# Performance work log

Measured on AMD Instinct MI355X. Metric: run time of the kernel, lower is better.

The kernel has to match this reference:

```python
import jax, jax.numpy as jnp
import numpy as np

B, N, CS, CZ, CH, H, PQ, PV = 1, 768, 384, 128, 16, 12, 4, 8
INF, EPS, LN_EPS = 1e5, 1e-8, 1e-5


def setup_inputs() -> dict:
    key = jax.random.key(0)
    ks = jax.random.split(key, 16)
    def nrm(k, shape, scale=0.02):
        return jax.random.normal(k, shape, dtype=jnp.float32) * scale
    return {
        "s": jax.random.normal(ks[0], (B, N, CS), jnp.float32),
        "z": jax.random.normal(ks[1], (B, N, N, CZ), jnp.float32),
        "r_rot": jax.random.normal(ks[2], (B, N, 5, 3, 3), jnp.float32),
        "r_trans": jax.random.normal(ks[3], (B, N, 5, 3), jnp.float32),
        "mask": jnp.ones((B, N, 5), jnp.float32),
        "wq": nrm(ks[4], (H * CH, CS)), "bq": jnp.zeros((H * CH,), jnp.float32),
        "wkv": nrm(ks[5], (2 * H * CH, CS)), "bkv": jnp.zeros((2 * H * CH,), jnp.float32),
        "wqp": nrm(ks[6], (H * PQ * 3, CS)), "bqp": jnp.zeros((H * PQ * 3,), jnp.float32),
        "wkvp": nrm(ks[7], (H * (PQ + PV) * 3, CS)), "bkvp": jnp.zeros((H * (PQ + PV) * 3,), jnp.float32),
        "wb": nrm(ks[8], (H, CZ)), "bb": jnp.zeros((H,), jnp.float32),
        "head_w": nrm(ks[9], (H,), 0.5),
        "wout": nrm(ks[10], (CS, H * (CZ + CH + PV * 4))), "bout": jnp.zeros((CS,), jnp.float32),
        "wexp": nrm(ks[11], (5 * CS, CS)), "bexp": jnp.zeros((5 * CS,), jnp.float32),
        "ln_g": jnp.ones((CS,), jnp.float32), "ln_b": jnp.zeros((CS,), jnp.float32),
        "ww": nrm(ks[12], (1, CS)), "bw": jnp.zeros((1,), jnp.float32),
    }


def _mix(x, fg_mask, weight, ndims):
    # x: [B,N,5,...]; weighted blend of backbone frame (index 0) and mean of
    # masked functional-group frames (indices 1:5).
    bb_f = x[:, :, :1]
    m = fg_mask.reshape(fg_mask.shape + (1,) * ndims)
    fg = (x[:, :, 1:] * m).sum(axis=2, keepdims=True)
    denom = fg_mask.sum(-1, keepdims=True).reshape(fg_mask.shape[:2] + (1,) * (ndims + 1))
    fg = fg / (denom + 1e-8)
    w = weight.reshape(weight.shape[:2] + (1,) * (ndims + 1))
    return (w * bb_f + (1.0 - w) * fg)[:, :, 0]


def _ipa(s, z, r_rot, r_trans, mask, wq, bq, wkv, bkv, wqp, bqp, wkvp, bkvp,
         wb, bb, head_w, wout, bout, wexp, bexp, ln_g, ln_b, ww, bw):
    fg_mask = mask[..., 1:]            # [B,N,4]
    ulr = mask[..., 0]                 # [B,N]
    # softmax over a size-1 axis (as in original code -> all ones)
    weight = jax.nn.softmax(s @ ww.T + bw, axis=-1)   # [B,N,1]

    se = (s @ wexp.T + bexp).reshape(B, N, 5, CS)
    mu = se.mean(-1, keepdims=True)
    var = ((se - mu) ** 2).mean(-1, keepdims=True)
    se = (se - mu) * jax.lax.rsqrt(var + LN_EPS) * ln_g + ln_b

    q = _mix((se @ wq.T + bq).reshape(B, N, 5, H, CH), fg_mask, weight, 2)      # [B,N,H,CH]
    kv = _mix((se @ wkv.T + bkv).reshape(B, N, 5, H, 2 * CH), fg_mask, weight, 2)
    k, v = kv[..., :CH], kv[..., CH:]

    def pts_of(w_, b_, npts):
        lin = se @ w_.T + b_                                   # [B,N,5,3*H*npts]
        pts = jnp.moveaxis(lin.reshape(B, N, 5, 3, H * npts), -2, -1)  # [B,N,5,H*npts,3]
        pts = jnp.einsum('bnfij,bnfpj->bnfpi', r_rot, pts) + r_trans[:, :, :, None, :]
        return _mix(pts.reshape(B, N, 5, H, npts, 3), fg_mask, weight, 3)

    q_pts = pts_of(wqp, bqp, PQ)                               # [B,N,H,PQ,3]
    kv_pts = pts_of(wkvp, bkvp, PQ + PV)
    k_pts, v_pts = kv_pts[..., :PQ, :], kv_pts[..., PQ:, :]

    bias = z @ wb.T + bb                                       # [B,N,N,H]
    a = jnp.einsum('bihc,bjhc->bhij', q, k) * (1.0 / (3 * CH)) ** 0.5
    a = a + (1.0 / 3.0) ** 0.5 * jnp.transpose(bias, (0, 3, 1, 2))

    d2 = jnp.sum((q_pts[:, :, None] - k_pts[:, None]) ** 2, axis=-1)  # [B,N,N,H,PQ]
    hw = jax.nn.softplus(head_w) * (1.0 / (3 * (PQ * 9.0 / 2))) ** 0.5
    pt_att = -0.5 * jnp.sum(d2 * hw[:, None], axis=-1)         # [B,N,N,H]
    a = a + jnp.transpose(pt_att, (0, 3, 1, 2))
    sq_mask = INF * (ulr[:, :, None] * ulr[:, None, :] - 1.0)
    a = jax.nn.softmax(a + sq_mask[:, None], axis=-1)          # [B,H,N,N]

    o = jnp.einsum('bhij,bjhc->bihc', a, v).reshape(B, N, H * CH)
    o_pt = jnp.einsum('bhij,bjhpx->bihpx', a, v_pts)           # [B,N,H,PV,3]
    rot0, t0 = r_rot[:, :, 0], r_trans[:, :, 0]                # backbone frame
    # invert_apply: R^T (x - t)
    o_pt = jnp.einsum('bnik,bnhpi->bnhpk', rot0, o_pt - t0[:, :, None, None, :])
    o_pt_norm = jnp.sqrt(jnp.sum(o_pt ** 2, -1) + EPS).reshape(B, N, H * PV)
    o_pt = o_pt.reshape(B, N, H * PV, 3)
    o_pair = jnp.einsum('bhij,bijc->bihc', a, z).reshape(B, N, H * CZ)
    cat = jnp.concatenate([o, o_pt[..., 0], o_pt[..., 1], o_pt[..., 2], o_pt_norm, o_pair], -1)
    return cat @ wout.T + bout                                 # [B,N,CS]


def reference(s, z, r_rot, r_trans, mask, wq, bq, wkv, bkv, wqp, bqp, wkvp, bkvp,
              wb, bb, head_w, wout, bout, wexp, bexp, ln_g, ln_b, ww, bw):
    return _ipa(s, z, r_rot, r_trans, mask, wq, bq, wkv, bkv, wqp, bqp, wkvp, bkvp,
                wb, bb, head_w, wout, bout, wexp, bexp, ln_g, ln_b, ww, bw)
```

## Files before the change

### kernel.cpp

```cpp
#include <hip/hip_runtime.h>
#include <hip/hip_bf16.h>
#include <stdint.h>


typedef float  f32x4 __attribute__((ext_vector_type(4)));
typedef short  s16x8 __attribute__((ext_vector_type(8)));

__device__ __forceinline__ float bf2f(unsigned short u) {
    union { unsigned int i; float f; } v; v.i = ((unsigned int)u) << 16; return v.f;
}
__device__ __forceinline__ unsigned short f2bf(float f) {
    union { float f; unsigned int i; } v; v.f = f;
    unsigned int r = v.i + 0x7fffu + ((v.i >> 16) & 1u);
    return (unsigned short)(r >> 16);
}
__device__ __forceinline__ unsigned packbf2(float a, float b) {
    return (unsigned)f2bf(a) | ((unsigned)f2bf(b) << 16);
}
__device__ __forceinline__ float bval(int c,
    const float* bq, const float* bkv, const float* bqp, const float* bkvp)
{
    if (c < 192)      return bq[c];
    else if (c < 576) return bkv[c - 192];
    else if (c < 720) return bqp[c - 576];
    else              return bkvp[c - 720];
}

__global__ __launch_bounds__(256) void k_prep(
    const float* __restrict__ s, const float* __restrict__ wexp,
    const float* __restrict__ wq, const float* __restrict__ wkv,
    const float* __restrict__ wqp, const float* __restrict__ wkvp,
    const float* __restrict__ wout,
    const float* __restrict__ bq, const float* __restrict__ bkv,
    const float* __restrict__ bqp, const float* __restrict__ bkvp,
    unsigned short* __restrict__ s_bf, unsigned short* __restrict__ we_bf,
    unsigned short* __restrict__ wc_bf, unsigned short* __restrict__ wo_bf,
    float* __restrict__ bcat)
{
    const int x = blockIdx.x * 256 + threadIdx.x;
    if (x >= 1696896) return;
    if (x < 294912)            s_bf[x] = f2bf(s[x]);
    else if (x < 442368)       we_bf[x - 294912] = f2bf(wexp[x - 294912]);
    else if (x < 516096)       wc_bf[x - 442368] = f2bf(wq[x - 442368]);
    else if (x < 663552)       wc_bf[73728 + (x - 516096)] = f2bf(wkv[x - 516096]);
    else if (x < 718848)       wc_bf[221184 + (x - 663552)] = f2bf(wqp[x - 663552]);
    else if (x < 884736)       wc_bf[276480 + (x - 718848)] = f2bf(wkvp[x - 718848]);
    else if (x < 1695744)      wo_bf[x - 884736] = f2bf(wout[x - 884736]);
    else {
        int j = x - 1695744;
        bcat[j] = bval(j, bq, bkv, bqp, bkvp);
    }
}

__global__ __launch_bounds__(256) void k_mm(
    const unsigned short* __restrict__ A, int lda,
    const unsigned short* __restrict__ B, int ldb,
    float* __restrict__ C, int ldc, const float* __restrict__ bias,
    int nk, size_t pstride)
{
    const int m0 = blockIdx.x * 64, n0 = blockIdx.y * 64;
    const int koff = blockIdx.z * nk * 32;
    C += (size_t)blockIdx.z * pstride;
    const int t = threadIdx.x;
    const int lane = t & 63, wave = t >> 6, quad = lane >> 4, lcol = lane & 15;
    const int mh = (wave & 1) * 32, nh = (wave >> 1) * 32;
    __shared__ unsigned short As[64 * 40];
    __shared__ unsigned short Bs[64 * 40];
    const int lr = t >> 2, ls = (t & 3) * 8;
    const unsigned short* Ap = A + (size_t)(m0 + lr) * lda + koff + ls;
    const unsigned short* Bp = B + (size_t)(n0 + lr) * ldb + koff + ls;
    f32x4 acc[2][2] = {};

    uint4 av = *(const uint4*)Ap;
    uint4 bv = *(const uint4*)Bp;
    for (int kc = 0; kc < nk; ++kc) {
        __syncthreads();
        *(uint4*)&As[lr * 40 + ls] = av;
        *(uint4*)&Bs[lr * 40 + ls] = bv;
        __syncthreads();
        if (kc + 1 < nk) {
            av = *(const uint4*)(Ap + (size_t)(kc + 1) * 32);
            bv = *(const uint4*)(Bp + (size_t)(kc + 1) * 32);
        }
        s16x8 af0 = *(const s16x8*)&As[(mh + lcol) * 40 + quad * 8];
        s16x8 af1 = *(const s16x8*)&As[(mh + 16 + lcol) * 40 + quad * 8];
        s16x8 bf0 = *(const s16x8*)&Bs[(nh + lcol) * 40 + quad * 8];
        s16x8 bf1 = *(const s16x8*)&Bs[(nh + 16 + lcol) * 40 + quad * 8];
        acc[0][0] = __builtin_amdgcn_mfma_f32_16x16x32_bf16(af0, bf0, acc[0][0], 0, 0, 0);
        acc[0][1] = __builtin_amdgcn_mfma_f32_16x16x32_bf16(af0, bf1, acc[0][1], 0, 0, 0);
        acc[1][0] = __builtin_amdgcn_mfma_f32_16x16x32_bf16(af1, bf0, acc[1][0], 0, 0, 0);
        acc[1][1] = __builtin_amdgcn_mfma_f32_16x16x32_bf16(af1, bf1, acc[1][1], 0, 0, 0);
    }
    #pragma unroll
    for (int r = 0; r < 2; ++r)
        #pragma unroll
        for (int c = 0; c < 2; ++c) {
            int gn = n0 + nh + c * 16 + lcol;
            float bv2 = bias ? bias[gn] : 0.f;
            #pragma unroll
            for (int ii = 0; ii < 4; ++ii) {
                int gm = m0 + mh + r * 16 + quad * 4 + ii;
                C[(size_t)gm * ldc + gn] = acc[r][c][ii] + bv2;
            }
        }
}

__global__ __launch_bounds__(256) void k_ln(
    const float* __restrict__ se_raw, const float* __restrict__ ln_g,
    const float* __restrict__ ln_b, unsigned short* __restrict__ se0_bf)
{
    const int n = blockIdx.x * 4 + (threadIdx.x >> 6);
    const int lane = threadIdx.x & 63;
    const float* row = se_raw + (size_t)n * 384;
    float v[6], s1 = 0.f, s2 = 0.f;
    #pragma unroll
    for (int q = 0; q < 6; ++q) {
        v[q] = row[lane + q * 64];
        s1 += v[q]; s2 += v[q] * v[q];
    }
    for (int mk = 1; mk < 64; mk <<= 1) {
        s1 += __shfl_xor(s1, mk, 64);
        s2 += __shfl_xor(s2, mk, 64);
    }
    float mu = s1 * (1.f / 384.f);
    float var = s2 * (1.f / 384.f) - mu * mu;
    float rs = rsqrtf(fmaxf(var, 0.f) + 1e-5f);
    unsigned short* orow = se0_bf + (size_t)n * 384;
    #pragma unroll
    for (int q = 0; q < 6; ++q) {
        int c = lane + q * 64;
        orow[c] = f2bf((v[q] - mu) * rs * ln_g[c] + ln_b[c]);
    }
}

__global__ __launch_bounds__(256) void k_post(
    const float* __restrict__ lin,
    const float* __restrict__ r_rot, const float* __restrict__ r_trans,
    float* __restrict__ q_out, unsigned short* __restrict__ k_out,
    unsigned short* __restrict__ v_out, float* __restrict__ qp_out,
    unsigned short* __restrict__ kp_out, unsigned short* __restrict__ vp_out,
    float* __restrict__ k2_out)
{
    const int n0 = blockIdx.x * 8;
    const int t = threadIdx.x;
    __shared__ float kprot[8 * 144];

    for (int r = 0; r < 8; ++r) {
        const int n = n0 + r;
        const float* lrow = lin + (size_t)n * 1152;
        const float* rot = r_rot + (size_t)n * 45;
        for (int u = t; u < 1152; u += 256) {
            if (u < 192) {
                q_out[(size_t)n * 192 + u] = lrow[u];
            } else if (u < 576) {
                int l2 = u - 192, h = l2 >> 5, c = l2 & 31;
                float v = lrow[u];
                if (c < 16) k_out[(size_t)n * 192 + h * 16 + c] = f2bf(v);
                else        v_out[(size_t)n * 192 + h * 16 + (c - 16)] = f2bf(v);
            } else {
                int y = u - 576;
                int pt = y / 3, i = y - pt * 3;
                float t0 = r_trans[(size_t)n * 15 + i];
                float v;
                if (pt < 48) {
                    v = rot[i*3+0] * lrow[576 + pt]
                      + rot[i*3+1] * lrow[576 + 48 + pt]
                      + rot[i*3+2] * lrow[576 + 96 + pt] + t0;
                    qp_out[(size_t)n * 144 + pt * 3 + i] = v;
                } else {
                    int pp = pt - 48;
                    v = rot[i*3+0] * lrow[720 + pp]
                      + rot[i*3+1] * lrow[720 + 144 + pp]
                      + rot[i*3+2] * lrow[720 + 288 + pp] + t0;
                    int h = pp / 12, pl = pp - h * 12;
                    if (pl < 4) {
                        kp_out[(size_t)n * 144 + (h * 4 + pl) * 3 + i] = f2bf(v);
                        kprot[r * 144 + (h * 4 + pl) * 3 + i] = v;
                    } else {
                        vp_out[(size_t)n * 288 + (h * 8 + (pl - 4)) * 3 + i] = f2bf(v);
                    }
                }
            }
        }
    }
    __syncthreads();
    if (t < 96) {
        int r = t / 12, h = t - r * 12;
        float ss = 0.f;
        #pragma unroll
        for (int d = 0; d < 12; ++d) {
            float v = kprot[r * 144 + h * 12 + d];
            ss += v * v;
        }
        k2_out[(size_t)(n0 + r) * 12 + h] = ss;
    }
}

__global__ __launch_bounds__(256) void k_attn(
    const float* __restrict__ z, const float* __restrict__ mask,
    const float* __restrict__ head_w, const float* __restrict__ wb,
    const float* __restrict__ bb,
    const float* __restrict__ r_rot, const float* __restrict__ r_trans,
    const float* __restrict__ q_ws, const float* __restrict__ qp_ws,
    const float* __restrict__ k2_ws,
    const unsigned short* __restrict__ k_bf, const unsigned short* __restrict__ v_bf,
    const unsigned short* __restrict__ kp_bf, const unsigned short* __restrict__ vp_bf,
    unsigned short* __restrict__ cat)
{
    const int i = blockIdx.x;
    const int t = threadIdx.x;
    const int lane = t & 63, wv = t >> 6;
    const int quad = lane >> 4, lcol = lane & 15;

    __shared__ short zb[64 * 136];
    __shared__ float L[64 * 17];
    __shared__ float Pt[16 * 68];
    __shared__ float qs[192], qps[144];
    __shared__ float ulra[768];
    __shared__ float m_s[16], l_s[16], alph_s[16], linv_s[16];
    __shared__ float optb[288];

    const float c_qk = 0.14433756729740643f;
    const float c_b  = 0.57735026918962576f;

    if (t < 192) qs[t]  = q_ws[(size_t)i * 192 + t];
    if (t < 144) qps[t] = qp_ws[(size_t)i * 144 + t];
    if (t >= 192 && t < 208) { int u = t - 192; m_s[u] = -1e30f; l_s[u] = 0.f; alph_s[u] = 1.f; }
    for (int x = t; x < 768; x += 256) ulra[x] = mask[(size_t)x * 5];
    for (int x = t; x < 4 * 68; x += 256) Pt[12 * 68 + x] = 0.f;
    const float ulr_i = mask[(size_t)i * 5];

    s16x8 wbf[4];
    #pragma unroll
    for (int kb = 0; kb < 4; ++kb) {
        #pragma unroll
        for (int j = 0; j < 8; ++j) {
            int c = kb * 32 + quad * 8 + j;
            wbf[kb][j] = (lcol < 12) ? (short)f2bf(wb[(size_t)lcol * 128 + c]) : (short)0;
        }
    }
    __syncthreads();

    const int hh = (lcol < 12) ? lcol : 11;
    f32x4 qv[4], qpv[3];
    float q2_r = 0.f;
    #pragma unroll
    for (int m = 0; m < 4; ++m) qv[m] = *(const f32x4*)&qs[hh * 16 + m * 4];
    #pragma unroll
    for (int m = 0; m < 3; ++m) {
        qpv[m] = *(const f32x4*)&qps[hh * 12 + m * 4];
        #pragma unroll
        for (int e = 0; e < 4; ++e) q2_r += qpv[m][e] * qpv[m][e];
    }
    float xh = head_w[hh];
    const float cpt_r = -0.5f * logf(1.f + __expf(xh)) * 0.13608276348795434f;
    const float cbb_r = c_b * bb[hh];

    f32x4 acc_op[2] = { {0.f,0.f,0.f,0.f}, {0.f,0.f,0.f,0.f} };
    f32x4 acc_s = {0.f,0.f,0.f,0.f};

    int vu = -1, vhalf = 0;
    if (t < 120) { vu = t; vhalf = 0; }
    else if (t >= 128 && t < 248) { vu = t - 128; vhalf = 1; }
    int vrole = -1; const unsigned int* vsrc = nullptr; int vstride = 0, voff = 0;
    if (vu >= 0) {
        if (vu < 48) { vrole = vu >> 2;       vsrc = (const unsigned int*)v_bf;  vstride = 96;  voff = vu * 2; }
        else         { vrole = (vu - 48) / 6; vsrc = (const unsigned int*)vp_bf; vstride = 144; voff = (vu - 48) * 2; }
    }

    const float* zbase = z + (size_t)i * 98304;
    f32x4 zr[8];
    #pragma unroll
    for (int sx = 0; sx < 8; ++sx)
        zr[sx] = *(const f32x4*)(zbase + (size_t)(t + sx * 256) * 4);

    const int jlb = wv * 16 + quad * 4;
    const int zrow = wv * 16 + lcol;
    const int sigm = (zrow >> 3) & 3;

    for (int tt = 0; tt < 12; ++tt) {
        const int j0 = tt * 64;
        __syncthreads();

        #pragma unroll
        for (int sx = 0; sx < 8; ++sx) {
            int idx = t + sx * 256;
            int jl = idx >> 5, cq = idx & 31;
            int ch = (cq >> 1) ^ ((jl >> 3) & 3);
            uint2 pk;
            pk.x = packbf2(zr[sx][0], zr[sx][1]);
            pk.y = packbf2(zr[sx][2], zr[sx][3]);
            *(uint2*)&zb[jl * 136 + ch * 8 + (cq & 1) * 4] = pk;
        }
        __syncthreads();

        if (tt < 11) {
            const float* znext = zbase + (size_t)(tt + 1) * 8192;
            #pragma unroll
            for (int sx = 0; sx < 8; ++sx)
                zr[sx] = *(const f32x4*)(znext + (size_t)(t + sx * 256) * 4);
        }
        uint4 ka[4], kb4[4]; uint2 p0[4], p1[4], p2[4]; float K2r[4];
        #pragma unroll
        for (int r = 0; r < 4; ++r) {
            int jr = j0 + jlb + r;
            const unsigned short* kr = k_bf + (size_t)jr * 192 + hh * 16;
            ka[r]  = *(const uint4*)kr;
            kb4[r] = *(const uint4*)(kr + 8);
            const unsigned short* pr = kp_bf + (size_t)jr * 144 + hh * 12;
            p0[r] = *(const uint2*)pr;
            p1[r] = *(const uint2*)(pr + 4);
            p2[r] = *(const uint2*)(pr + 8);
            K2r[r] = k2_ws[(size_t)jr * 12 + hh];
        }

        f32x4 d = {0.f, 0.f, 0.f, 0.f};
        #pragma unroll
        for (int kb = 0; kb < 4; ++kb) {
            s16x8 a = *(const s16x8*)&zb[zrow * 136 + ((kb * 4 + quad) ^ sigm) * 8];
            d = __builtin_amdgcn_mfma_f32_16x16x32_bf16(a, wbf[kb], d, 0, 0, 0);
        }

        if (lcol < 12) {
            #pragma unroll
            for (int r = 0; r < 4; ++r) {
                int jl = jlb + r;
                const unsigned* kwa = (const unsigned*)&ka[r];
                const unsigned* kwb = (const unsigned*)&kb4[r];
                float qk = 0.f;
                #pragma unroll
                for (int m = 0; m < 4; ++m) {
                    qk += qv[m >> 1][(m & 1) * 2 + 0] * bf2f((unsigned short)(kwa[m] & 0xffffu));
                    qk += qv[m >> 1][(m & 1) * 2 + 1] * bf2f((unsigned short)(kwa[m] >> 16));
                }
                #pragma unroll
                for (int m = 0; m < 4; ++m) {
                    qk += qv[2 + (m >> 1)][(m & 1) * 2 + 0] * bf2f((unsigned short)(kwb[m] & 0xffffu));
                    qk += qv[2 + (m >> 1)][(m & 1) * 2 + 1] * bf2f((unsigned short)(kwb[m] >> 16));
                }
                float dp = 0.f;
                dp += qpv[0][0] * bf2f((unsigned short)(p0[r].x & 0xffffu));
                dp += qpv[0][1] * bf2f((unsigned short)(p0[r].x >> 16));
                dp += qpv[0][2] * bf2f((unsigned short)(p0[r].y & 0xffffu));
                dp += qpv[0][3] * bf2f((unsigned short)(p0[r].y >> 16));
                dp += qpv[1][0] * bf2f((unsigned short)(p1[r].x & 0xffffu));
                dp += qpv[1][1] * bf2f((unsigned short)(p1[r].x >> 16));
                dp += qpv[1][2] * bf2f((unsigned short)(p1[r].y & 0xffffu));
                dp += qpv[1][3] * bf2f((unsigned short)(p1[r].y >> 16));
                dp += qpv[2][0] * bf2f((unsigned short)(p2[r].x & 0xffffu));
                dp += qpv[2][1] * bf2f((unsigned short)(p2[r].x >> 16));
                dp += qpv[2][2] * bf2f((unsigned short)(p2[r].y & 0xffffu));
                dp += qpv[2][3] * bf2f((unsigned short)(p2[r].y >> 16));
                float ptt = cpt_r * (q2_r + K2r[r] - 2.f * dp);
                float lg = c_qk * qk + ptt + 1e5f * (ulr_i * ulra[j0 + jl] - 1.f)
                         + c_b * d[r] + cbb_r;
                L[jl * 17 + lcol] = lg;
            }
        }
        __syncthreads();

        if (t < 192) {
            int h = t >> 4, u = t & 15;
            float v0 = L[(u * 4 + 0) * 17 + h];
            float v1 = L[(u * 4 + 1) * 17 + h];
            float v2 = L[(u * 4 + 2) * 17 + h];
            float v3 = L[(u * 4 + 3) * 17 + h];
            float mx = fmaxf(fmaxf(v0, v1), fmaxf(v2, v3));
            for (int mk = 1; mk < 16; mk <<= 1) mx = fmaxf(mx, __shfl_xor(mx, mk, 16));
            float mold = m_s[h];
            float mnew = fmaxf(mold, mx);
            float w0 = __expf(v0 - mnew), w1 = __expf(v1 - mnew);
            float w2 = __expf(v2 - mnew), w3 = __expf(v3 - mnew);
            Pt[h * 68 + u * 4 + 0] = w0;
            Pt[h * 68 + u * 4 + 1] = w1;
            Pt[h * 68 + u * 4 + 2] = w2;
            Pt[h * 68 + u * 4 + 3] = w3;
            float sm = w0 + w1 + w2 + w3;
            for (int mk = 1; mk < 16; mk <<= 1) sm += __shfl_xor(sm, mk, 16);
            if (u == 0) {
                float al = __expf(mold - mnew);
                m_s[h] = mnew; alph_s[h] = al;
                l_s[h] = l_s[h] * al + sm;
            }
        }
        __syncthreads();

        {
            float al[4];
            #pragma unroll
            for (int r = 0; r < 4; ++r) al[r] = alph_s[quad * 4 + r];
            #pragma unroll
            for (int nt = 0; nt < 2; ++nt)
                #pragma unroll
                for (int r = 0; r < 4; ++r) acc_op[nt][r] *= al[r];
            #pragma unroll
            for (int kb = 0; kb < 2; ++kb) {
                f32x4 pa = *(const f32x4*)&Pt[lcol * 68 + kb * 32 + quad * 8];
                f32x4 pb = *(const f32x4*)&Pt[lcol * 68 + kb * 32 + quad * 8 + 4];
                union { s16x8 v; unsigned u[4]; } af;
                af.u[0] = packbf2(pa[0], pa[1]);
                af.u[1] = packbf2(pa[2], pa[3]);
                af.u[2] = packbf2(pb[0], pb[1]);
                af.u[3] = packbf2(pb[2], pb[3]);
                #pragma unroll
                for (int nt = 0; nt < 2; ++nt) {
                    int c = wv * 32 + nt * 16 + lcol;
                    int csw = ((c >> 3) ^ quad) * 8 + (c & 7);
                    s16x8 bfg;
                    #pragma unroll
                    for (int j = 0; j < 8; ++j)
                        bfg[j] = zb[(kb * 32 + quad * 8 + j) * 136 + csw];
                    acc_op[nt] = __builtin_amdgcn_mfma_f32_16x16x32_bf16(af.v, bfg, acc_op[nt], 0, 0, 0);
                }
            }
        }
        if (vu >= 0) {
            float alpha = alph_s[vrole];
            f32x4 a = acc_s;
            a[0] *= alpha; a[1] *= alpha; a[2] *= alpha; a[3] *= alpha;
            const float* prow = &Pt[vrole * 68 + vhalf * 32];
            const unsigned int* src = vsrc + (size_t)(j0 + vhalf * 32) * vstride + voff;
            #pragma unroll 4
            for (int jj = 0; jj < 32; jj += 4) {
                f32x4 p = *(const f32x4*)(prow + jj);
                #pragma unroll
                for (int m = 0; m < 4; ++m) {
                    uint2 w = *(const uint2*)(src + (size_t)(jj + m) * vstride);
                    float pm = p[m];
                    a[0] += pm * bf2f((unsigned short)(w.x & 0xffffu));
                    a[1] += pm * bf2f((unsigned short)(w.x >> 16));
                    a[2] += pm * bf2f((unsigned short)(w.y & 0xffffu));
                    a[3] += pm * bf2f((unsigned short)(w.y >> 16));
                }
            }
            acc_s = a;
        }
    }

    __syncthreads();
    if (t < 16) linv_s[t] = (t < 12) ? 1.f / l_s[t] : 0.f;
    float* vbuf = L;
    if (vu >= 0) {
        #pragma unroll
        for (int m = 0; m < 4; ++m) vbuf[(vu * 2 + vhalf) * 4 + m] = acc_s[m];
    }
    __syncthreads();
    unsigned short* crow = cat + (size_t)i * 2112;
    if (t < 120) {
        int role = (t < 48) ? (t >> 2) : (t - 48) / 6;
        float li = linv_s[role];
        float f[4];
        #pragma unroll
        for (int m = 0; m < 4; ++m)
            f[m] = (vbuf[(t * 2) * 4 + m] + vbuf[(t * 2 + 1) * 4 + m]) * li;
        if (t < 48) {
            #pragma unroll
            for (int m = 0; m < 4; ++m) crow[t * 4 + m] = f2bf(f[m]);
        } else {
            int e0 = (t - 48) * 4;
            optb[e0 + 0] = f[0]; optb[e0 + 1] = f[1];
            optb[e0 + 2] = f[2]; optb[e0 + 3] = f[3];
        }
    }
    {
        #pragma unroll
        for (int nt = 0; nt < 2; ++nt)
            #pragma unroll
            for (int r = 0; r < 4; ++r) {
                int h = quad * 4 + r;
                if (h < 12)
                    crow[576 + h * 128 + wv * 32 + nt * 16 + lcol] = f2bf(acc_op[nt][r] * linv_s[h]);
            }
    }
    __syncthreads();
    if (t < 96) {
        int hp = t;
        const float* rot = r_rot + (size_t)i * 45;
        float d0 = optb[hp * 3 + 0] - r_trans[(size_t)i * 15 + 0];
        float d1 = optb[hp * 3 + 1] - r_trans[(size_t)i * 15 + 1];
        float d2 = optb[hp * 3 + 2] - r_trans[(size_t)i * 15 + 2];
        float f0 = rot[0] * d0 + rot[3] * d1 + rot[6] * d2;
        float f1 = rot[1] * d0 + rot[4] * d1 + rot[7] * d2;
        float f2 = rot[2] * d0 + rot[5] * d1 + rot[8] * d2;
        crow[192 + hp] = f2bf(f0);
        crow[288 + hp] = f2bf(f1);
        crow[384 + hp] = f2bf(f2);
        crow[480 + hp] = f2bf(sqrtf(f0 * f0 + f1 * f1 + f2 * f2 + 1e-8f));
    }
}

__global__ __launch_bounds__(256) void k_out_red(
    const float* __restrict__ parts, const float* __restrict__ bout,
    float* __restrict__ out)
{
    const int x = blockIdx.x * 256 + threadIdx.x;
    float s = bout[x % 384];
    #pragma unroll
    for (int p = 0; p < 6; ++p) s += parts[(size_t)p * 294912 + x];
    out[x] = s;
}

extern "C" void kernel_launch(void* const* d_in, const int* in_sizes, int n_in,
                              void* d_out, int out_size, void* d_ws, size_t ws_size,
                              hipStream_t stream)
{
    const float* s       = (const float*)d_in[0];
    const float* z       = (const float*)d_in[1];
    const float* r_rot   = (const float*)d_in[2];
    const float* r_trans = (const float*)d_in[3];
    const float* mask    = (const float*)d_in[4];
    const float* wq      = (const float*)d_in[5];
    const float* bq      = (const float*)d_in[6];
    const float* wkv     = (const float*)d_in[7];
    const float* bkv     = (const float*)d_in[8];
    const float* wqp     = (const float*)d_in[9];
    const float* bqp     = (const float*)d_in[10];
    const float* wkvp    = (const float*)d_in[11];
    const float* bkvp    = (const float*)d_in[12];
    const float* wb      = (const float*)d_in[13];
    const float* bb      = (const float*)d_in[14];
    const float* head_w  = (const float*)d_in[15];
    const float* wout    = (const float*)d_in[16];
    const float* bout    = (const float*)d_in[17];
    const float* wexp    = (const float*)d_in[18];
    const float* bexp    = (const float*)d_in[19];
    const float* ln_g    = (const float*)d_in[20];
    const float* ln_b    = (const float*)d_in[21];

    float* wsf = (float*)d_ws;
    float* se_raw = wsf;
    float* lin    = wsf + 294912;
    float* qf     = wsf + 1179648;
    float* qpf    = wsf + 1327104;
    float* k2w    = wsf + 1437696;
    float* bcat   = wsf + 1446912;
    float* parts  = wsf + 1448064;
    unsigned short* ub = (unsigned short*)(wsf + 3217536);
    unsigned short* s_bf   = ub;
    unsigned short* we_bf  = ub + 294912;
    unsigned short* wc_bf  = ub + 442368;
    unsigned short* wo_bf  = ub + 884736;
    unsigned short* se0_bf = ub + 1695744;
    unsigned short* kbf    = ub + 1990656;
    unsigned short* vbf    = ub + 2138112;
    unsigned short* kpbf   = ub + 2285568;
    unsigned short* vpbf   = ub + 2396160;
    unsigned short* cat_bf = ub + 2617344;
    float* out = (float*)d_out;

    k_prep<<<6629, 256, 0, stream>>>(s, wexp, wq, wkv, wqp, wkvp, wout,
                                     bq, bkv, bqp, bkvp,
                                     s_bf, we_bf, wc_bf, wo_bf, bcat);
    k_mm<<<dim3(12, 6, 1), 256, 0, stream>>>(s_bf, 384, we_bf, 384,
                                             se_raw, 384, bexp, 12, 0);
    k_ln<<<192, 256, 0, stream>>>(se_raw, ln_g, ln_b, se0_bf);
    k_mm<<<dim3(12, 18, 1), 256, 0, stream>>>(se0_bf, 384, wc_bf, 384,
                                              lin, 1152, bcat, 12, 0);
    k_post<<<96, 256, 0, stream>>>(lin, r_rot, r_trans,
                                   qf, kbf, vbf, qpf, kpbf, vpbf, k2w);
    k_attn<<<768, 256, 0, stream>>>(z, mask, head_w, wb, bb, r_rot, r_trans,
                                    qf, qpf, k2w, kbf, vbf, kpbf, vpbf, cat_bf);
    k_mm<<<dim3(12, 6, 6), 256, 0, stream>>>(cat_bf, 2112, wo_bf, 2112,
                                             parts, 384, nullptr, 11, 294912);
    k_out_red<<<1152, 256, 0, stream>>>(parts, bout, out);
}
```

Baseline: 556.9 us.

## Store K/V/point intermediates in fp32 and load them lazily in attention

K, V, key points and value points are now written as fp32 instead of bf16, which removes the bf16 unpacking ALU work in the attention kernel. The K and key-point loads are no longer prefetched into registers before the z-tile staging. They are loaded per row inside a non-unrolled loop, and launch_bounds asks for 3 blocks per SM to cut register pressure and raise occupancy. In exchange the gathered K/V data doubles in size and global-load latency is exposed inside the score loop.

```diff
diff --git a/kernel.cpp b/kernel.cpp
--- a/kernel.cpp
+++ b/kernel.cpp
@@ -136,9 +136,9 @@
 __global__ __launch_bounds__(256) void k_post(
     const float* __restrict__ lin,
     const float* __restrict__ r_rot, const float* __restrict__ r_trans,
-    float* __restrict__ q_out, unsigned short* __restrict__ k_out,
-    unsigned short* __restrict__ v_out, float* __restrict__ qp_out,
-    unsigned short* __restrict__ kp_out, unsigned short* __restrict__ vp_out,
+    float* __restrict__ q_out, float* __restrict__ k_out,
+    float* __restrict__ v_out, float* __restrict__ qp_out,
+    float* __restrict__ kp_out, float* __restrict__ vp_out,
     float* __restrict__ k2_out)
 {
     const int n0 = blockIdx.x * 8;
@@ -155,8 +155,8 @@
             } else if (u < 576) {
                 int l2 = u - 192, h = l2 >> 5, c = l2 & 31;
                 float v = lrow[u];
-                if (c < 16) k_out[(size_t)n * 192 + h * 16 + c] = f2bf(v);
-                else        v_out[(size_t)n * 192 + h * 16 + (c - 16)] = f2bf(v);
+                if (c < 16) k_out[(size_t)n * 192 + h * 16 + c] = v;
+                else        v_out[(size_t)n * 192 + h * 16 + (c - 16)] = v;
             } else {
                 int y = u - 576;
                 int pt = y / 3, i = y - pt * 3;
@@ -174,10 +174,10 @@
                       + rot[i*3+2] * lrow[720 + 288 + pp] + t0;
                     int h = pp / 12, pl = pp - h * 12;
                     if (pl < 4) {
-                        kp_out[(size_t)n * 144 + (h * 4 + pl) * 3 + i] = f2bf(v);
+                        kp_out[(size_t)n * 144 + (h * 4 + pl) * 3 + i] = v;
                         kprot[r * 144 + (h * 4 + pl) * 3 + i] = v;
                     } else {
-                        vp_out[(size_t)n * 288 + (h * 8 + (pl - 4)) * 3 + i] = f2bf(v);
+                        vp_out[(size_t)n * 288 + (h * 8 + (pl - 4)) * 3 + i] = v;
                     }
                 }
             }
@@ -196,15 +196,15 @@
     }
 }
 
-__global__ __launch_bounds__(256) void k_attn(
+__global__ __launch_bounds__(256, 3) void k_attn(
     const float* __restrict__ z, const float* __restrict__ mask,
     const float* __restrict__ head_w, const float* __restrict__ wb,
     const float* __restrict__ bb,
     const float* __restrict__ r_rot, const float* __restrict__ r_trans,
     const float* __restrict__ q_ws, const float* __restrict__ qp_ws,
     const float* __restrict__ k2_ws,
-    const unsigned short* __restrict__ k_bf, const unsigned short* __restrict__ v_bf,
-    const unsigned short* __restrict__ kp_bf, const unsigned short* __restrict__ vp_bf,
+    const float* __restrict__ k_f, const float* __restrict__ v_f,
+    const float* __restrict__ kp_f, const float* __restrict__ vp_f,
     unsigned short* __restrict__ cat)
 {
     const int i = blockIdx.x;
@@ -262,10 +262,10 @@
     int vu = -1, vhalf = 0;
     if (t < 120) { vu = t; vhalf = 0; }
     else if (t >= 128 && t < 248) { vu = t - 128; vhalf = 1; }
-    int vrole = -1; const unsigned int* vsrc = nullptr; int vstride = 0, voff = 0;
+    int vrole = -1; const float* vsrc = nullptr; int vstride = 0, voff = 0;
     if (vu >= 0) {
-        if (vu < 48) { vrole = vu >> 2;       vsrc = (const unsigned int*)v_bf;  vstride = 96;  voff = vu * 2; }
-        else         { vrole = (vu - 48) / 6; vsrc = (const unsigned int*)vp_bf; vstride = 144; voff = (vu - 48) * 2; }
+        if (vu < 48) { vrole = vu >> 2;       vsrc = v_f;  vstride = 192; voff = vu * 4; }
+        else         { vrole = (vu - 48) / 6; vsrc = vp_f; vstride = 288; voff = (vu - 48) * 4; }
     }
 
     const float* zbase = z + (size_t)i * 98304;
@@ -300,19 +300,6 @@
             for (int sx = 0; sx < 8; ++sx)
                 zr[sx] = *(const f32x4*)(znext + (size_t)(t + sx * 256) * 4);
         }
-        uint4 ka[4], kb4[4]; uint2 p0[4], p1[4], p2[4]; float K2r[4];
-        #pragma unroll
-        for (int r = 0; r < 4; ++r) {
-            int jr = j0 + jlb + r;
-            const unsigned short* kr = k_bf + (size_t)jr * 192 + hh * 16;
-            ka[r]  = *(const uint4*)kr;
-            kb4[r] = *(const uint4*)(kr + 8);
-            const unsigned short* pr = kp_bf + (size_t)jr * 144 + hh * 12;
-            p0[r] = *(const uint2*)pr;
-            p1[r] = *(const uint2*)(pr + 4);
-            p2[r] = *(const uint2*)(pr + 8);
-            K2r[r] = k2_ws[(size_t)jr * 12 + hh];
-        }
 
         f32x4 d = {0.f, 0.f, 0.f, 0.f};
         #pragma unroll
@@ -322,39 +309,34 @@
         }
 
         if (lcol < 12) {
-            #pragma unroll
+            #pragma unroll 1
             for (int r = 0; r < 4; ++r) {
-                int jl = jlb + r;
-                const unsigned* kwa = (const unsigned*)&ka[r];
-                const unsigned* kwb = (const unsigned*)&kb4[r];
-                float qk = 0.f;
+                const int jr = j0 + jlb + r;
+                const float* kr = k_f + (size_t)jr * 192 + hh * 16;
+                const float* pr = kp_f + (size_t)jr * 144 + hh * 12;
+                f32x4 k0 = *(const f32x4*)(kr + 0);
+                f32x4 k1 = *(const f32x4*)(kr + 4);
+                f32x4 k2 = *(const f32x4*)(kr + 8);
+                f32x4 k3 = *(const f32x4*)(kr + 12);
+                f32x4 p0 = *(const f32x4*)(pr + 0);
+                f32x4 p1 = *(const f32x4*)(pr + 4);
+                f32x4 p2 = *(const f32x4*)(pr + 8);
+                float K2v = k2_ws[(size_t)jr * 12 + hh];
+                float qk = 0.f, dp = 0.f;
                 #pragma unroll
-                for (int m = 0; m < 4; ++m) {
-                    qk += qv[m >> 1][(m & 1) * 2 + 0] * bf2f((unsigned short)(kwa[m] & 0xffffu));
-                    qk += qv[m >> 1][(m & 1) * 2 + 1] * bf2f((unsigned short)(kwa[m] >> 16));
+                for (int e = 0; e < 4; ++e) {
+                    qk += qv[0][e] * k0[e];
+                    qk += qv[1][e] * k1[e];
+                    qk += qv[2][e] * k2[e];
+                    qk += qv[3][e] * k3[e];
+                    dp += qpv[0][e] * p0[e];
+                    dp += qpv[1][e] * p1[e];
+                    dp += qpv[2][e] * p2[e];
                 }
-                #pragma unroll
-                for (int m = 0; m < 4; ++m) {
-                    qk += qv[2 + (m >> 1)][(m & 1) * 2 + 0] * bf2f((unsigned short)(kwb[m] & 0xffffu));
-                    qk += qv[2 + (m >> 1)][(m & 1) * 2 + 1] * bf2f((unsigned short)(kwb[m] >> 16));
-                }
-                float dp = 0.f;
-                dp += qpv[0][0] * bf2f((unsigned short)(p0[r].x & 0xffffu));
-                dp += qpv[0][1] * bf2f((unsigned short)(p0[r].x >> 16));
-                dp += qpv[0][2] * bf2f((unsigned short)(p0[r].y & 0xffffu));
-                dp += qpv[0][3] * bf2f((unsigned short)(p0[r].y >> 16));
-                dp += qpv[1][0] * bf2f((unsigned short)(p1[r].x & 0xffffu));
-                dp += qpv[1][1] * bf2f((unsigned short)(p1[r].x >> 16));
-                dp += qpv[1][2] * bf2f((unsigned short)(p1[r].y & 0xffffu));
-                dp += qpv[1][3] * bf2f((unsigned short)(p1[r].y >> 16));
-                dp += qpv[2][0] * bf2f((unsigned short)(p2[r].x & 0xffffu));
-                dp += qpv[2][1] * bf2f((unsigned short)(p2[r].x >> 16));
-                dp += qpv[2][2] * bf2f((unsigned short)(p2[r].y & 0xffffu));
-                dp += qpv[2][3] * bf2f((unsigned short)(p2[r].y >> 16));
-                float ptt = cpt_r * (q2_r + K2r[r] - 2.f * dp);
-                float lg = c_qk * qk + ptt + 1e5f * (ulr_i * ulra[j0 + jl] - 1.f)
+                float ptt = cpt_r * (q2_r + K2v - 2.f * dp);
+                float lg = c_qk * qk + ptt + 1e5f * (ulr_i * ulra[j0 + jlb + r] - 1.f)
                          + c_b * d[r] + cbb_r;
-                L[jl * 17 + lcol] = lg;
+                L[(jlb + r) * 17 + lcol] = lg;
             }
         }
         __syncthreads();
@@ -419,18 +401,18 @@
             f32x4 a = acc_s;
             a[0] *= alpha; a[1] *= alpha; a[2] *= alpha; a[3] *= alpha;
             const float* prow = &Pt[vrole * 68 + vhalf * 32];
-            const unsigned int* src = vsrc + (size_t)(j0 + vhalf * 32) * vstride + voff;
+            const float* src = vsrc + (size_t)(j0 + vhalf * 32) * vstride + voff;
             #pragma unroll 4
             for (int jj = 0; jj < 32; jj += 4) {
                 f32x4 p = *(const f32x4*)(prow + jj);
                 #pragma unroll
                 for (int m = 0; m < 4; ++m) {
-                    uint2 w = *(const uint2*)(src + (size_t)(jj + m) * vstride);
+                    f32x4 w = *(const f32x4*)(src + (size_t)(jj + m) * vstride);
                     float pm = p[m];
-                    a[0] += pm * bf2f((unsigned short)(w.x & 0xffffu));
-                    a[1] += pm * bf2f((unsigned short)(w.x >> 16));
-                    a[2] += pm * bf2f((unsigned short)(w.y & 0xffffu));
-                    a[3] += pm * bf2f((unsigned short)(w.y >> 16));
+                    a[0] += pm * w[0];
+                    a[1] += pm * w[1];
+                    a[2] += pm * w[2];
+                    a[3] += pm * w[3];
                 }
             }
             acc_s = a;
@@ -535,17 +517,17 @@
     float* k2w    = wsf + 1437696;
     float* bcat   = wsf + 1446912;
     float* parts  = wsf + 1448064;
-    unsigned short* ub = (unsigned short*)(wsf + 3217536);
+    float* kf     = wsf + 3217536;
+    float* vf     = wsf + 3364992;
+    float* kpf    = wsf + 3512448;
+    float* vpf    = wsf + 3623040;
+    unsigned short* ub = (unsigned short*)(wsf + 3844224);
     unsigned short* s_bf   = ub;
     unsigned short* we_bf  = ub + 294912;
     unsigned short* wc_bf  = ub + 442368;
     unsigned short* wo_bf  = ub + 884736;
     unsigned short* se0_bf = ub + 1695744;
-    unsigned short* kbf    = ub + 1990656;
-    unsigned short* vbf    = ub + 2138112;
-    unsigned short* kpbf   = ub + 2285568;
-    unsigned short* vpbf   = ub + 2396160;
-    unsigned short* cat_bf = ub + 2617344;
+    unsigned short* cat_bf = ub + 1990656;
     float* out = (float*)d_out;
 
     k_prep<<<6629, 256, 0, stream>>>(s, wexp, wq, wkv, wqp, wkvp, wout,
@@ -557,9 +539,9 @@
     k_mm<<<dim3(12, 18, 1), 256, 0, stream>>>(se0_bf, 384, wc_bf, 384,
                                               lin, 1152, bcat, 12, 0);
     k_post<<<96, 256, 0, stream>>>(lin, r_rot, r_trans,
-                                   qf, kbf, vbf, qpf, kpbf, vpbf, k2w);
+                                   qf, kf, vf, qpf, kpf, vpf, k2w);
     k_attn<<<768, 256, 0, stream>>>(z, mask, head_w, wb, bb, r_rot, r_trans,
-                                    qf, qpf, k2w, kbf, vbf, kpbf, vpbf, cat_bf);
+                                    qf, qpf, k2w, kf, vf, kpf, vpf, cat_bf);
     k_mm<<<dim3(12, 6, 6), 256, 0, stream>>>(cat_bf, 2112, wo_bf, 2112,
                                              parts, 384, nullptr, 11, 294912);
     k_out_red<<<1152, 256, 0, stream>>>(parts, bout, out);
```

After: 590.8 us. 6.1% more time.

## Double-buffer z tiles in LDS and keep V/VP values in fp32

Applied to the files above, without the earlier changes.

The attention kernel now keeps two LDS buffers for the bf16-packed z tile. The next tile is converted and stored after the softmax stage, which removes one barrier per iteration and overlaps the global prefetch with compute. V and V-point values are stored and read as fp32 instead of bf16, which drops the unpack work but doubles their bandwidth. The kernel also gets a launch-bounds occupancy hint of 3 and reads q directly from global, at the cost of more LDS use and register pressure.

```diff
diff --git a/kernel.cpp b/kernel.cpp
--- a/kernel.cpp
+++ b/kernel.cpp
@@ -137,8 +137,8 @@
     const float* __restrict__ lin,
     const float* __restrict__ r_rot, const float* __restrict__ r_trans,
     float* __restrict__ q_out, unsigned short* __restrict__ k_out,
-    unsigned short* __restrict__ v_out, float* __restrict__ qp_out,
-    unsigned short* __restrict__ kp_out, unsigned short* __restrict__ vp_out,
+    float* __restrict__ v_out, float* __restrict__ qp_out,
+    unsigned short* __restrict__ kp_out, float* __restrict__ vp_out,
     float* __restrict__ k2_out)
 {
     const int n0 = blockIdx.x * 8;
@@ -156,7 +156,7 @@
                 int l2 = u - 192, h = l2 >> 5, c = l2 & 31;
                 float v = lrow[u];
                 if (c < 16) k_out[(size_t)n * 192 + h * 16 + c] = f2bf(v);
-                else        v_out[(size_t)n * 192 + h * 16 + (c - 16)] = f2bf(v);
+                else        v_out[(size_t)n * 192 + h * 16 + (c - 16)] = v;
             } else {
                 int y = u - 576;
                 int pt = y / 3, i = y - pt * 3;
@@ -177,7 +177,7 @@
                         kp_out[(size_t)n * 144 + (h * 4 + pl) * 3 + i] = f2bf(v);
                         kprot[r * 144 + (h * 4 + pl) * 3 + i] = v;
                     } else {
-                        vp_out[(size_t)n * 288 + (h * 8 + (pl - 4)) * 3 + i] = f2bf(v);
+                        vp_out[(size_t)n * 288 + (h * 8 + (pl - 4)) * 3 + i] = v;
                     }
                 }
             }
@@ -196,15 +196,15 @@
     }
 }
 
-__global__ __launch_bounds__(256) void k_attn(
+__global__ __launch_bounds__(256, 3) void k_attn(
     const float* __restrict__ z, const float* __restrict__ mask,
     const float* __restrict__ head_w, const float* __restrict__ wb,
     const float* __restrict__ bb,
     const float* __restrict__ r_rot, const float* __restrict__ r_trans,
     const float* __restrict__ q_ws, const float* __restrict__ qp_ws,
     const float* __restrict__ k2_ws,
-    const unsigned short* __restrict__ k_bf, const unsigned short* __restrict__ v_bf,
-    const unsigned short* __restrict__ kp_bf, const unsigned short* __restrict__ vp_bf,
+    const unsigned short* __restrict__ k_bf, const float* __restrict__ v_f,
+    const unsigned short* __restrict__ kp_bf, const float* __restrict__ vp_f,
     unsigned short* __restrict__ cat)
 {
     const int i = blockIdx.x;
@@ -212,7 +212,7 @@
     const int lane = t & 63, wv = t >> 6;
     const int quad = lane >> 4, lcol = lane & 15;
 
-    __shared__ short zb[64 * 136];
+    __shared__ short zb[2][64 * 136];
     __shared__ float L[64 * 17];
     __shared__ float Pt[16 * 68];
     __shared__ float qs[192], qps[144];
@@ -239,18 +239,21 @@
             wbf[kb][j] = (lcol < 12) ? (short)f2bf(wb[(size_t)lcol * 128 + c]) : (short)0;
         }
     }
-    __syncthreads();
 
     const int hh = (lcol < 12) ? lcol : 11;
     f32x4 qv[4], qpv[3];
     float q2_r = 0.f;
-    #pragma unroll
-    for (int m = 0; m < 4; ++m) qv[m] = *(const f32x4*)&qs[hh * 16 + m * 4];
-    #pragma unroll
-    for (int m = 0; m < 3; ++m) {
-        qpv[m] = *(const f32x4*)&qps[hh * 12 + m * 4];
-        #pragma unroll
-        for (int e = 0; e < 4; ++e) q2_r += qpv[m][e] * qpv[m][e];
+    {
+        const float* qg  = q_ws  + (size_t)i * 192 + hh * 16;
+        const float* qpg = qp_ws + (size_t)i * 144 + hh * 12;
+        #pragma unroll
+        for (int m = 0; m < 4; ++m) qv[m] = *(const f32x4*)(qg + m * 4);
+        #pragma unroll
+        for (int m = 0; m < 3; ++m) {
+            qpv[m] = *(const f32x4*)(qpg + m * 4);
+            #pragma unroll
+            for (int e = 0; e < 4; ++e) q2_r += qpv[m][e] * qpv[m][e];
+        }
     }
     float xh = head_w[hh];
     const float cpt_r = -0.5f * logf(1.f + __expf(xh)) * 0.13608276348795434f;
@@ -262,44 +265,40 @@
     int vu = -1, vhalf = 0;
     if (t < 120) { vu = t; vhalf = 0; }
     else if (t >= 128 && t < 248) { vu = t - 128; vhalf = 1; }
-    int vrole = -1; const unsigned int* vsrc = nullptr; int vstride = 0, voff = 0;
+    int vrole = -1; const float* vsrc = nullptr; int vstride = 0, voff = 0;
     if (vu >= 0) {
-        if (vu < 48) { vrole = vu >> 2;       vsrc = (const unsigned int*)v_bf;  vstride = 96;  voff = vu * 2; }
-        else         { vrole = (vu - 48) / 6; vsrc = (const unsigned int*)vp_bf; vstride = 144; voff = (vu - 48) * 2; }
-    }
-
-    const float* zbase = z + (size_t)i * 98304;
-    f32x4 zr[8];
-    #pragma unroll
-    for (int sx = 0; sx < 8; ++sx)
-        zr[sx] = *(const f32x4*)(zbase + (size_t)(t + sx * 256) * 4);
+        if (vu < 48) { vrole = vu >> 2;       vsrc = v_f;  vstride = 192; voff = vu * 4; }
+        else         { vrole = (vu - 48) / 6; vsrc = vp_f; vstride = 288; voff = (vu - 48) * 4; }
+    }
 
     const int jlb = wv * 16 + quad * 4;
     const int zrow = wv * 16 + lcol;
     const int sigm = (zrow >> 3) & 3;
 
+    const float* zbase = z + (size_t)i * 98304;
+    f32x4 zr[8];
+    #pragma unroll
+    for (int sx = 0; sx < 8; ++sx)
+        zr[sx] = *(const f32x4*)(zbase + (size_t)(t + sx * 256) * 4);
+    #pragma unroll
+    for (int sx = 0; sx < 8; ++sx) {
+        int idx = t + sx * 256;
+        int jl = idx >> 5, cq = idx & 31;
+        int ch = (cq >> 1) ^ ((jl >> 3) & 3);
+        uint2 pk;
+        pk.x = packbf2(zr[sx][0], zr[sx][1]);
+        pk.y = packbf2(zr[sx][2], zr[sx][3]);
+        *(uint2*)&zb[0][jl * 136 + ch * 8 + (cq & 1) * 4] = pk;
+    }
+    #pragma unroll
+    for (int sx = 0; sx < 8; ++sx)
+        zr[sx] = *(const f32x4*)(zbase + 8192 + (size_t)(t + sx * 256) * 4);
+    __syncthreads();
+
+    int cur = 0;
     for (int tt = 0; tt < 12; ++tt) {
         const int j0 = tt * 64;
-        __syncthreads();
-
-        #pragma unroll
-        for (int sx = 0; sx < 8; ++sx) {
-            int idx = t + sx * 256;
-            int jl = idx >> 5, cq = idx & 31;
-            int ch = (cq >> 1) ^ ((jl >> 3) & 3);
-            uint2 pk;
-            pk.x = packbf2(zr[sx][0], zr[sx][1]);
-            pk.y = packbf2(zr[sx][2], zr[sx][3]);
-            *(uint2*)&zb[jl * 136 + ch * 8 + (cq & 1) * 4] = pk;
-        }
-        __syncthreads();
-
-        if (tt < 11) {
-            const float* znext = zbase + (size_t)(tt + 1) * 8192;
-            #pragma unroll
-            for (int sx = 0; sx < 8; ++sx)
-                zr[sx] = *(const f32x4*)(znext + (size_t)(t + sx * 256) * 4);
-        }
+
         uint4 ka[4], kb4[4]; uint2 p0[4], p1[4], p2[4]; float K2r[4];
         #pragma unroll
         for (int r = 0; r < 4; ++r) {
@@ -317,7 +316,7 @@
         f32x4 d = {0.f, 0.f, 0.f, 0.f};
         #pragma unroll
         for (int kb = 0; kb < 4; ++kb) {
-            s16x8 a = *(const s16x8*)&zb[zrow * 136 + ((kb * 4 + quad) ^ sigm) * 8];
+            s16x8 a = *(const s16x8*)&zb[cur][zrow * 136 + ((kb * 4 + quad) ^ sigm) * 8];
             d = __builtin_amdgcn_mfma_f32_16x16x32_bf16(a, wbf[kb], d, 0, 0, 0);
         }
 
@@ -383,6 +382,24 @@
                 l_s[h] = l_s[h] * al + sm;
             }
         }
+        if (tt < 11) {
+            #pragma unroll
+            for (int sx = 0; sx < 8; ++sx) {
+                int idx = t + sx * 256;
+                int jl = idx >> 5, cq = idx & 31;
+                int ch = (cq >> 1) ^ ((jl >> 3) & 3);
+                uint2 pk;
+                pk.x = packbf2(zr[sx][0], zr[sx][1]);
+                pk.y = packbf2(zr[sx][2], zr[sx][3]);
+                *(uint2*)&zb[cur ^ 1][jl * 136 + ch * 8 + (cq & 1) * 4] = pk;
+            }
+            if (tt < 10) {
+                const float* znext = zbase + (size_t)(tt + 2) * 8192;
+                #pragma unroll
+                for (int sx = 0; sx < 8; ++sx)
+                    zr[sx] = *(const f32x4*)(znext + (size_t)(t + sx * 256) * 4);
+            }
+        }
         __syncthreads();
 
         {
@@ -409,7 +426,7 @@
                     s16x8 bfg;
                     #pragma unroll
                     for (int j = 0; j < 8; ++j)
-                        bfg[j] = zb[(kb * 32 + quad * 8 + j) * 136 + csw];
+                        bfg[j] = zb[cur][(kb * 32 + quad * 8 + j) * 136 + csw];
                     acc_op[nt] = __builtin_amdgcn_mfma_f32_16x16x32_bf16(af.v, bfg, acc_op[nt], 0, 0, 0);
                 }
             }
@@ -419,22 +436,23 @@
             f32x4 a = acc_s;
             a[0] *= alpha; a[1] *= alpha; a[2] *= alpha; a[3] *= alpha;
             const float* prow = &Pt[vrole * 68 + vhalf * 32];
-            const unsigned int* src = vsrc + (size_t)(j0 + vhalf * 32) * vstride + voff;
+            const float* src = vsrc + (size_t)(j0 + vhalf * 32) * vstride + voff;
             #pragma unroll 4
             for (int jj = 0; jj < 32; jj += 4) {
                 f32x4 p = *(const f32x4*)(prow + jj);
                 #pragma unroll
                 for (int m = 0; m < 4; ++m) {
-                    uint2 w = *(const uint2*)(src + (size_t)(jj + m) * vstride);
+                    f32x4 w = *(const f32x4*)(src + (size_t)(jj + m) * vstride);
                     float pm = p[m];
-                    a[0] += pm * bf2f((unsigned short)(w.x & 0xffffu));
-                    a[1] += pm * bf2f((unsigned short)(w.x >> 16));
-                    a[2] += pm * bf2f((unsigned short)(w.y & 0xffffu));
-                    a[3] += pm * bf2f((unsigned short)(w.y >> 16));
+                    a[0] += pm * w[0];
+                    a[1] += pm * w[1];
+                    a[2] += pm * w[2];
+                    a[3] += pm * w[3];
                 }
             }
             acc_s = a;
         }
+        if (tt < 11) cur ^= 1;
     }
 
     __syncthreads();
@@ -535,17 +553,17 @@
     float* k2w    = wsf + 1437696;
     float* bcat   = wsf + 1446912;
     float* parts  = wsf + 1448064;
-    unsigned short* ub = (unsigned short*)(wsf + 3217536);
+    float* vf     = wsf + 3217536;
+    float* vpf    = wsf + 3364992;
+    unsigned short* ub = (unsigned short*)(wsf + 3586176);
     unsigned short* s_bf   = ub;
     unsigned short* we_bf  = ub + 294912;
     unsigned short* wc_bf  = ub + 442368;
     unsigned short* wo_bf  = ub + 884736;
     unsigned short* se0_bf = ub + 1695744;
     unsigned short* kbf    = ub + 1990656;
-    unsigned short* vbf    = ub + 2138112;
-    unsigned short* kpbf   = ub + 2285568;
-    unsigned short* vpbf   = ub + 2396160;
-    unsigned short* cat_bf = ub + 2617344;
+    unsigned short* kpbf   = ub + 2138112;
+    unsigned short* cat_bf = ub + 2248704;
     float* out = (float*)d_out;
 
     k_prep<<<6629, 256, 0, stream>>>(s, wexp, wq, wkv, wqp, wkvp, wout,
@@ -557,9 +575,9 @@
     k_mm<<<dim3(12, 18, 1), 256, 0, stream>>>(se0_bf, 384, wc_bf, 384,
                                               lin, 1152, bcat, 12, 0);
     k_post<<<96, 256, 0, stream>>>(lin, r_rot, r_trans,
-                                   qf, kbf, vbf, qpf, kpbf, vpbf, k2w);
+                                   qf, kbf, vf, qpf, kpbf, vpf, k2w);
     k_attn<<<768, 256, 0, stream>>>(z, mask, head_w, wb, bb, r_rot, r_trans,
-                                    qf, qpf, k2w, kbf, vbf, kpbf, vpbf, cat_bf);
+                                    qf, qpf, k2w, kbf, vf, kpbf, vpf, cat_bf);
     k_mm<<<dim3(12, 6, 6), 256, 0, stream>>>(cat_bf, 2112, wo_bf, 2112,
                                              parts, 384, nullptr, 11, 294912);
     k_out_red<<<1152, 256, 0, stream>>>(parts, bout, out);
```

After: 642.3 us. 1.15x slower.
